# Kernel tuning notes

Hardware: AMD Instinct MI355X
Metric: run time of the kernel (lower is better)

## Reference

```python
import jax, jax.numpy as jnp
import numpy as np

N_NODES = 100000
N_EDGES = 1000000
HIDDEN = 128
GROUPS = [[0, 1, 2], [3, 4, 5], [6, 7, 8]]  # model_ids[i]['volume_ids']
COMBOS = [(0, 0), (0, 1), (0, 2), (1, 1), (1, 2), (2, 2)]  # combinations with replacement
LN_EPS = 1e-5


def _ln(h, g, b):
    m = jnp.mean(h, axis=-1, keepdims=True)
    v = jnp.var(h, axis=-1, keepdims=True)
    return (h - m) * jax.lax.rsqrt(v + LN_EPS) * g + b


def setup_inputs() -> dict:
    key = jax.random.key(0)
    ks = jax.random.split(key, 8)
    C = len(COMBOS)
    s = 0.02
    x = jax.random.normal(ks[0], (N_NODES, HIDDEN), jnp.float32)
    e = jax.random.normal(ks[1], (N_EDGES, HIDDEN), jnp.float32)
    edge_index = jax.random.randint(ks[2], (2, N_EDGES), 0, N_NODES)
    volume_id = jax.random.randint(ks[3], (N_NODES,), 0, 9)
    W1 = (jax.random.normal(ks[4], (C, 3 * HIDDEN, HIDDEN), jnp.float32) * s)
    b1 = jnp.zeros((C, HIDDEN), jnp.float32)
    g1 = jnp.ones((C, HIDDEN), jnp.float32)
    be1 = jnp.zeros((C, HIDDEN), jnp.float32)
    W2 = (jax.random.normal(ks[5], (C, HIDDEN, HIDDEN), jnp.float32) * s)
    b2 = jnp.zeros((C, HIDDEN), jnp.float32)
    g2 = jnp.ones((C, HIDDEN), jnp.float32)
    be2 = jnp.zeros((C, HIDDEN), jnp.float32)
    W3 = (jax.random.normal(ks[6], (C, HIDDEN, 1), jnp.float32) * s)
    b3 = jnp.zeros((C, 1), jnp.float32)
    return dict(x=x, edge_index=edge_index, e=e, volume_id=volume_id,
                W1=W1, b1=b1, g1=g1, be1=be1,
                W2=W2, b2=b2, g2=g2, be2=be2,
                W3=W3, b3=b3)


def reference(x, edge_index, e, volume_id, W1, b1, g1, be1, W2, b2, g2, be2, W3, b3):
    # volume id -> group id lookup (constant, from hparams['model_ids'])
    group_of_vol = np.zeros(9, dtype=np.int32)
    for gi, vols in enumerate(GROUPS):
        group_of_vol[vols] = gi
    group_of_vol = jnp.asarray(group_of_vol)

    start, end = edge_index[0], edge_index[1]
    gs = group_of_vol[volume_id[start]]  # [E] group of start node
    ge = group_of_vol[volume_id[end]]    # [E] group of end node
    xs = x[start]                        # [E, H] gather
    xe = x[end]                          # [E, H] gather

    out = jnp.zeros((start.shape[0], 1), x.dtype)
    for c, (ga, gb) in enumerate(COMBOS):
        mask = (gs == ga) & (ge == gb)   # torch.isin on disjoint volume groups
        # split first Linear to avoid materializing concat([xs, xe, e])
        h = xs @ W1[c, :HIDDEN] + xe @ W1[c, HIDDEN:2 * HIDDEN] + e @ W1[c, 2 * HIDDEN:] + b1[c]
        h = jax.nn.relu(_ln(h, g1[c], be1[c]))
        h = jax.nn.relu(_ln(h @ W2[c] + b2[c], g2[c], be2[c]))
        logit = h @ W3[c] + b3[c]        # [E, 1]
        out = jnp.where(mask[:, None], logit, out)  # masked scatter into shared buffer
    return out
```

## Files before the change

### kernel.cpp

```cpp
#include <hip/hip_runtime.h>

#define E_EDGES 1000000
#define N_NODES 100000
#define HID 128

static constexpr int    WS_CMB  = 256;
static constexpr int    WS_LIST = 1000448;
static constexpr int    WS_W1F  = 5001984;
static constexpr int    WS_W2F  = 5591808;

typedef __bf16 bf16x8 __attribute__((ext_vector_type(8)));
typedef float  f32x4  __attribute__((ext_vector_type(4)));

__device__ __forceinline__ unsigned short f2bf(float f) {
    unsigned int u = __builtin_bit_cast(unsigned int, f);
    u = (u + 0x7FFFu + ((u >> 16) & 1u)) >> 16;
    return (unsigned short)u;
}

__global__ void k_wconv(const float* __restrict__ W1, const float* __restrict__ W2,
                        unsigned short* __restrict__ w1f, unsigned short* __restrict__ w2f) {
    int idx = blockIdx.x * 256 + threadIdx.x;
    if (idx < 294912) {
        int j = idx & 7, lane = (idx >> 3) & 63, nt = (idx >> 9) & 7;
        int t = idx >> 12;
        int c = t / 12, kt = t - c * 12;
        int k = kt * 32 + ((lane >> 4) << 3) + j;
        int n = (nt << 4) + (lane & 15);
        w1f[idx] = f2bf(W1[(c * 384 + k) * 128 + n]);
    } else {
        int i2 = idx - 294912;
        int j = i2 & 7, lane = (i2 >> 3) & 63, nt = (i2 >> 9) & 7;
        int t = i2 >> 12;
        int c = t >> 2, kt = t & 3;
        int k = kt * 32 + ((lane >> 4) << 3) + j;
        int n = (nt << 4) + (lane & 15);
        w2f[i2] = f2bf(W2[(c * 128 + k) * 128 + n]);
    }
}

__global__ void k_classify(const int* __restrict__ ei, const int* __restrict__ vol,
                           signed char* __restrict__ cmb, float* __restrict__ out,
                           int* __restrict__ counts) {
    __shared__ int bc[6];
    int tid = threadIdx.x;
    if (tid < 6) bc[tid] = 0;
    __syncthreads();
    int eid = blockIdx.x * 256 + tid;
    if (eid < E_EDGES) {
        int s = ei[eid], t = ei[E_EDGES + eid];
        int gs = vol[s] / 3, ge = vol[t] / 3;
        int cc = -1;
        if (gs <= ge) cc = (gs == 0 ? 0 : (gs == 1 ? 2 : 3)) + ge;
        cmb[eid] = (signed char)cc;
        if (cc < 0) out[eid] = 0.f;
        else atomicAdd(&bc[cc], 1);
    }
    __syncthreads();
    if (tid < 6 && bc[tid] > 0) atomicAdd(&counts[tid], bc[tid]);
}

__global__ void k_offsets(int* __restrict__ ws) {
    if (threadIdx.x == 0 && blockIdx.x == 0) {
        int* counts = ws;
        int* seg    = ws + 16;
        int* tile   = ws + 24;
        int acc = 0;
        for (int c = 0; c < 6; ++c) {
            seg[c]  = acc;
            tile[c] = acc >> 6;
            acc += ((counts[c] + 63) >> 6) << 6;
        }
        seg[6]  = acc;
        tile[6] = acc >> 6;
    }
}

__global__ void k_scatter(const signed char* __restrict__ cmb, int* __restrict__ list,
                          const int* __restrict__ seg, int* __restrict__ cursor) {
    __shared__ int bc[6], basep[6];
    int tid = threadIdx.x;
    if (tid < 6) bc[tid] = 0;
    __syncthreads();
    int eid = blockIdx.x * 256 + tid;
    int cc = -1, lp = 0;
    if (eid < E_EDGES) {
        cc = cmb[eid];
        if (cc >= 0) lp = atomicAdd(&bc[cc], 1);
    }
    __syncthreads();
    if (tid < 6) basep[tid] = bc[tid] > 0 ? atomicAdd(&cursor[tid], bc[tid]) : 0;
    __syncthreads();
    if (cc >= 0) list[seg[cc] + basep[cc] + lp] = eid;
}

__global__ __launch_bounds__(256) void k_mlp(
    const float* __restrict__ x, const int* __restrict__ ei, const float* __restrict__ efeat,
    const int* __restrict__ tile_tab, const int* __restrict__ list,
    const unsigned short* __restrict__ w1f, const unsigned short* __restrict__ w2f,
    const float* __restrict__ b1, const float* __restrict__ g1, const float* __restrict__ be1,
    const float* __restrict__ b2, const float* __restrict__ g2, const float* __restrict__ be2,
    const float* __restrict__ W3, const float* __restrict__ b3,
    float* __restrict__ out)
{
    __shared__ unsigned short Albuf[64 * 392];
    __shared__ int eids_s[64], sn[64], en[64];

    int b = blockIdx.x;
    if (b >= tile_tab[6]) return;
    int c = 0;
#pragma unroll
    for (int k = 1; k < 6; ++k) if (b >= tile_tab[k]) c = k;
    int tb = b - tile_tab[c];
    int segbase = tile_tab[c] * 64;
    int tid = threadIdx.x;

    if (tid < 64) {
        int eid = list[segbase + tb * 64 + tid];
        eids_s[tid] = eid;
        int a = 0, bb = 0;
        if (eid >= 0) { a = ei[eid]; bb = ei[E_EDGES + eid]; }
        sn[tid] = a; en[tid] = bb;
    }
    __syncthreads();

#pragma unroll
    for (int sec = 0; sec < 3; ++sec) {
#pragma unroll
        for (int it = 0; it < 8; ++it) {
            int i = tid + it * 256;
            int r = i >> 5, c4 = i & 31;
            float4 v = make_float4(0.f, 0.f, 0.f, 0.f);
            if (eids_s[r] >= 0) {
                const float* src;
                if (sec == 0)      src = x + (long)sn[r] * 128;
                else if (sec == 1) src = x + (long)en[r] * 128;
                else               src = efeat + (long)eids_s[r] * 128;
                v = ((const float4*)src)[c4];
            }
            ushort4 u;
            u.x = f2bf(v.x); u.y = f2bf(v.y); u.z = f2bf(v.z); u.w = f2bf(v.w);
            *(ushort4*)(&Albuf[r * 392 + sec * 128 + c4 * 4]) = u;
        }
    }
    __syncthreads();

    int lane = tid & 63;
    int wv = tid >> 6;
    int colb = lane & 15;
    int quad = lane >> 4;

    const bf16x8* w1v = (const bf16x8*)w1f;
    const bf16x8* w2v = (const bf16x8*)w2f;
    const f32x4 zero4 = {0.f, 0.f, 0.f, 0.f};

    f32x4 acc[8];
#pragma unroll
    for (int nt = 0; nt < 8; ++nt) acc[nt] = zero4;
    int arow = (wv * 16 + colb) * 392 + quad * 8;
#pragma unroll
    for (int kt = 0; kt < 12; ++kt) {
        bf16x8 af = *(const bf16x8*)(&Albuf[arow + kt * 32]);
        int wbase = ((c * 12 + kt) * 8) * 64 + lane;
#pragma unroll
        for (int nt = 0; nt < 8; ++nt) {
            bf16x8 bf = w1v[wbase + nt * 64];
            acc[nt] = __builtin_amdgcn_mfma_f32_16x16x32_bf16(af, bf, acc[nt], 0, 0, 0);
        }
    }

    float pb[8], pg[8], pe[8];
#pragma unroll
    for (int nt = 0; nt < 8; ++nt) {
        int col = c * 128 + colb + nt * 16;
        pb[nt] = b1[col]; pg[nt] = g1[col]; pe[nt] = be1[col];
    }
    float sum[4] = {0, 0, 0, 0}, sq[4] = {0, 0, 0, 0};
#pragma unroll
    for (int nt = 0; nt < 8; ++nt)
#pragma unroll
        for (int r = 0; r < 4; ++r) {
            float v = acc[nt][r] + pb[nt];
            acc[nt][r] = v;
            sum[r] += v; sq[r] += v * v;
        }
#pragma unroll
    for (int m = 1; m < 16; m <<= 1)
#pragma unroll
        for (int r = 0; r < 4; ++r) {
            sum[r] += __shfl_xor(sum[r], m);
            sq[r]  += __shfl_xor(sq[r], m);
        }
    float mean_[4], rstd_[4];
#pragma unroll
    for (int r = 0; r < 4; ++r) {
        float mu = sum[r] * 0.0078125f;
        float var = sq[r] * 0.0078125f - mu * mu;
        mean_[r] = mu;
        rstd_[r] = rsqrtf(var + 1e-5f);
    }
    int h1base = wv * 6272;
#pragma unroll
    for (int nt = 0; nt < 8; ++nt)
#pragma unroll
        for (int r = 0; r < 4; ++r) {
            float v = (acc[nt][r] - mean_[r]) * rstd_[r] * pg[nt] + pe[nt];
            v = fmaxf(v, 0.f);
            Albuf[h1base + (quad * 4 + r) * 136 + colb + nt * 16] = f2bf(v);
        }

    f32x4 acc2[8];
#pragma unroll
    for (int nt = 0; nt < 8; ++nt) acc2[nt] = zero4;
    int h1row = wv * 6272 + colb * 136 + quad * 8;
#pragma unroll
    for (int kt = 0; kt < 4; ++kt) {
        bf16x8 af = *(const bf16x8*)(&Albuf[h1row + kt * 32]);
        int wbase = ((c * 4 + kt) * 8) * 64 + lane;
#pragma unroll
        for (int nt = 0; nt < 8; ++nt) {
            bf16x8 bf = w2v[wbase + nt * 64];
            acc2[nt] = __builtin_amdgcn_mfma_f32_16x16x32_bf16(af, bf, acc2[nt], 0, 0, 0);
        }
    }

#pragma unroll
    for (int nt = 0; nt < 8; ++nt) {
        int col = c * 128 + colb + nt * 16;
        pb[nt] = b2[col]; pg[nt] = g2[col]; pe[nt] = be2[col];
    }
#pragma unroll
    for (int r = 0; r < 4; ++r) { sum[r] = 0.f; sq[r] = 0.f; }
#pragma unroll
    for (int nt = 0; nt < 8; ++nt)
#pragma unroll
        for (int r = 0; r < 4; ++r) {
            float v = acc2[nt][r] + pb[nt];
            acc2[nt][r] = v;
            sum[r] += v; sq[r] += v * v;
        }
#pragma unroll
    for (int m = 1; m < 16; m <<= 1)
#pragma unroll
        for (int r = 0; r < 4; ++r) {
            sum[r] += __shfl_xor(sum[r], m);
            sq[r]  += __shfl_xor(sq[r], m);
        }
#pragma unroll
    for (int r = 0; r < 4; ++r) {
        float mu = sum[r] * 0.0078125f;
        float var = sq[r] * 0.0078125f - mu * mu;
        mean_[r] = mu;
        rstd_[r] = rsqrtf(var + 1e-5f);
    }
    float w3v[8];
#pragma unroll
    for (int nt = 0; nt < 8; ++nt) w3v[nt] = W3[c * 128 + colb + nt * 16];
    float part[4] = {0, 0, 0, 0};
#pragma unroll
    for (int nt = 0; nt < 8; ++nt)
#pragma unroll
        for (int r = 0; r < 4; ++r) {
            float v = (acc2[nt][r] - mean_[r]) * rstd_[r] * pg[nt] + pe[nt];
            v = fmaxf(v, 0.f);
            part[r] += v * w3v[nt];
        }
#pragma unroll
    for (int m = 1; m < 16; m <<= 1)
#pragma unroll
        for (int r = 0; r < 4; ++r) part[r] += __shfl_xor(part[r], m);

    float b3v = b3[c];
    if (colb == 0) {
#pragma unroll
        for (int r = 0; r < 4; ++r) {
            int eid = eids_s[wv * 16 + quad * 4 + r];
            if (eid >= 0) out[eid] = part[r] + b3v;
        }
    }
}

extern "C" void kernel_launch(void* const* d_in, const int* in_sizes, int n_in,
                              void* d_out, int out_size, void* d_ws, size_t ws_size,
                              hipStream_t stream) {
    const float* x    = (const float*)d_in[0];
    const int*   ei   = (const int*)d_in[1];
    const float* e    = (const float*)d_in[2];
    const int*   vol  = (const int*)d_in[3];
    const float* W1   = (const float*)d_in[4];
    const float* b1   = (const float*)d_in[5];
    const float* g1   = (const float*)d_in[6];
    const float* be1  = (const float*)d_in[7];
    const float* W2   = (const float*)d_in[8];
    const float* b2   = (const float*)d_in[9];
    const float* g2   = (const float*)d_in[10];
    const float* be2  = (const float*)d_in[11];
    const float* W3   = (const float*)d_in[12];
    const float* b3   = (const float*)d_in[13];
    float* out = (float*)d_out;
    char* wsb = (char*)d_ws;

    hipMemsetAsync(wsb, 0, 256, stream);
    hipMemsetAsync(wsb + WS_LIST, 0xFF, (E_EDGES + 384) * sizeof(int), stream);

    k_wconv<<<1536, 256, 0, stream>>>(W1, W2,
        (unsigned short*)(wsb + WS_W1F), (unsigned short*)(wsb + WS_W2F));
    k_classify<<<(E_EDGES + 255) / 256, 256, 0, stream>>>(ei, vol,
        (signed char*)(wsb + WS_CMB), out, (int*)wsb);
    k_offsets<<<1, 64, 0, stream>>>((int*)wsb);
    k_scatter<<<(E_EDGES + 255) / 256, 256, 0, stream>>>(
        (const signed char*)(wsb + WS_CMB), (int*)(wsb + WS_LIST),
        (const int*)(wsb + 64), (int*)(wsb + 32));
    k_mlp<<<E_EDGES / 64 + 6, 256, 0, stream>>>(
        x, ei, e, (const int*)(wsb + 96), (const int*)(wsb + WS_LIST),
        (const unsigned short*)(wsb + WS_W1F), (const unsigned short*)(wsb + WS_W2F),
        b1, g1, be1, b2, g2, be2, W3, b3, out);
}
```

Baseline: 1.080 ms.

## Load MLP input rows directly from global into MFMA fragments, shrink LDS

Removes the shared-memory staging of the gathered xs/xe/e rows. Each lane now reads its own edge's features straight from global memory into bf16 MFMA A-fragments, and LDS shrinks to the layer-1 output buffer alone. This drops two block-wide barriers and about 50KB of LDS per block, which should allow more resident blocks. The trade-off is less coalesced global loads, since each lane reads 32 bytes per row segment, and invalid edges now read row 0 rather than zeros.

```diff
diff --git a/kernel.cpp b/kernel.cpp
--- a/kernel.cpp
+++ b/kernel.cpp
@@ -103,8 +103,7 @@
     const float* __restrict__ W3, const float* __restrict__ b3,
     float* __restrict__ out)
 {
-    __shared__ unsigned short Albuf[64 * 392];
-    __shared__ int eids_s[64], sn[64], en[64];
+    __shared__ unsigned short H1[4 * 16 * 136];
 
     int b = blockIdx.x;
     if (b >= tile_tab[6]) return;
@@ -113,42 +112,20 @@
     for (int k = 1; k < 6; ++k) if (b >= tile_tab[k]) c = k;
     int tb = b - tile_tab[c];
     int segbase = tile_tab[c] * 64;
-    int tid = threadIdx.x;
-
-    if (tid < 64) {
-        int eid = list[segbase + tb * 64 + tid];
-        eids_s[tid] = eid;
-        int a = 0, bb = 0;
-        if (eid >= 0) { a = ei[eid]; bb = ei[E_EDGES + eid]; }
-        sn[tid] = a; en[tid] = bb;
-    }
-    __syncthreads();
-
-#pragma unroll
-    for (int sec = 0; sec < 3; ++sec) {
-#pragma unroll
-        for (int it = 0; it < 8; ++it) {
-            int i = tid + it * 256;
-            int r = i >> 5, c4 = i & 31;
-            float4 v = make_float4(0.f, 0.f, 0.f, 0.f);
-            if (eids_s[r] >= 0) {
-                const float* src;
-                if (sec == 0)      src = x + (long)sn[r] * 128;
-                else if (sec == 1) src = x + (long)en[r] * 128;
-                else               src = efeat + (long)eids_s[r] * 128;
-                v = ((const float4*)src)[c4];
-            }
-            ushort4 u;
-            u.x = f2bf(v.x); u.y = f2bf(v.y); u.z = f2bf(v.z); u.w = f2bf(v.w);
-            *(ushort4*)(&Albuf[r * 392 + sec * 128 + c4 * 4]) = u;
-        }
-    }
-    __syncthreads();
-
+
+    int tid  = threadIdx.x;
     int lane = tid & 63;
-    int wv = tid >> 6;
+    int wv   = tid >> 6;
     int colb = lane & 15;
     int quad = lane >> 4;
+
+    int eid  = list[segbase + tb * 64 + wv * 16 + colb];
+    int eidS = eid >= 0 ? eid : 0;
+    int s = ei[eidS], t = ei[E_EDGES + eidS];
+
+    const float* xs = x + (long)s * 128;
+    const float* xe = x + (long)t * 128;
+    const float* ee = efeat + (long)eidS * 128;
 
     const bf16x8* w1v = (const bf16x8*)w1f;
     const bf16x8* w2v = (const bf16x8*)w2f;
@@ -157,15 +134,21 @@
     f32x4 acc[8];
 #pragma unroll
     for (int nt = 0; nt < 8; ++nt) acc[nt] = zero4;
-    int arow = (wv * 16 + colb) * 392 + quad * 8;
+    int koff = quad * 8;
 #pragma unroll
     for (int kt = 0; kt < 12; ++kt) {
-        bf16x8 af = *(const bf16x8*)(&Albuf[arow + kt * 32]);
+        const float* src = (kt < 4) ? xs : ((kt < 8) ? xe : ee);
+        int o = (kt & 3) * 32 + koff;
+        float4 v0 = *(const float4*)(src + o);
+        float4 v1 = *(const float4*)(src + o + 4);
+        bf16x8 af;
+        af[0] = (__bf16)v0.x; af[1] = (__bf16)v0.y; af[2] = (__bf16)v0.z; af[3] = (__bf16)v0.w;
+        af[4] = (__bf16)v1.x; af[5] = (__bf16)v1.y; af[6] = (__bf16)v1.z; af[7] = (__bf16)v1.w;
         int wbase = ((c * 12 + kt) * 8) * 64 + lane;
 #pragma unroll
         for (int nt = 0; nt < 8; ++nt) {
-            bf16x8 bf = w1v[wbase + nt * 64];
-            acc[nt] = __builtin_amdgcn_mfma_f32_16x16x32_bf16(af, bf, acc[nt], 0, 0, 0);
+            bf16x8 bfr = w1v[wbase + nt * 64];
+            acc[nt] = __builtin_amdgcn_mfma_f32_16x16x32_bf16(af, bfr, acc[nt], 0, 0, 0);
         }
     }
 
@@ -199,28 +182,29 @@
         mean_[r] = mu;
         rstd_[r] = rsqrtf(var + 1e-5f);
     }
-    int h1base = wv * 6272;
+    int h1base = wv * 2176;
 #pragma unroll
     for (int nt = 0; nt < 8; ++nt)
 #pragma unroll
         for (int r = 0; r < 4; ++r) {
             float v = (acc[nt][r] - mean_[r]) * rstd_[r] * pg[nt] + pe[nt];
             v = fmaxf(v, 0.f);
-            Albuf[h1base + (quad * 4 + r) * 136 + colb + nt * 16] = f2bf(v);
+            H1[h1base + (quad * 4 + r) * 136 + colb + nt * 16] =
+                __builtin_bit_cast(unsigned short, (__bf16)v);
         }
 
     f32x4 acc2[8];
 #pragma unroll
     for (int nt = 0; nt < 8; ++nt) acc2[nt] = zero4;
-    int h1row = wv * 6272 + colb * 136 + quad * 8;
+    int h1row = wv * 2176 + colb * 136 + quad * 8;
 #pragma unroll
     for (int kt = 0; kt < 4; ++kt) {
-        bf16x8 af = *(const bf16x8*)(&Albuf[h1row + kt * 32]);
+        bf16x8 af = *(const bf16x8*)(&H1[h1row + kt * 32]);
         int wbase = ((c * 4 + kt) * 8) * 64 + lane;
 #pragma unroll
         for (int nt = 0; nt < 8; ++nt) {
-            bf16x8 bf = w2v[wbase + nt * 64];
-            acc2[nt] = __builtin_amdgcn_mfma_f32_16x16x32_bf16(af, bf, acc2[nt], 0, 0, 0);
+            bf16x8 bfr = w2v[wbase + nt * 64];
+            acc2[nt] = __builtin_amdgcn_mfma_f32_16x16x32_bf16(af, bfr, acc2[nt], 0, 0, 0);
         }
     }
 
@@ -271,12 +255,10 @@
         for (int r = 0; r < 4; ++r) part[r] += __shfl_xor(part[r], m);
 
     float b3v = b3[c];
-    if (colb == 0) {
-#pragma unroll
-        for (int r = 0; r < 4; ++r) {
-            int eid = eids_s[wv * 16 + quad * 4 + r];
-            if (eid >= 0) out[eid] = part[r] + b3v;
-        }
+#pragma unroll
+    for (int r = 0; r < 4; ++r) {
+        int esel = __shfl(eid, quad * 4 + r);
+        if (colb == 0 && esel >= 0) out[esel] = part[r] + b3v;
     }
 }
 
```

Result: no change. 1.069 ms (-1.1%).
